# Optimization experiments

Measured on AMD Instinct MI355X. Metric: run time of the kernel, lower is better.

The kernel has to match this reference:

```python
import jax, jax.numpy as jnp
import numpy as np

B, L, H, E = 4, 2048, 16, 64  # batch, seq, heads, head_dim (S=L, D=E)


def setup_inputs() -> dict:
    key = jax.random.key(0)
    kq, kk, kv = jax.random.split(key, 3)
    queries = jax.random.normal(kq, (B, L, H, E), dtype=jnp.float32)
    keys = jax.random.normal(kk, (B, L, H, E), dtype=jnp.float32)
    values = jax.random.normal(kv, (B, L, H, E), dtype=jnp.float32)
    return {"queries": queries, "keys": keys, "values": values}


def reference(queries, keys, values):
    Bq, Lq, Hq, Eq = queries.shape
    scale = 1.0 / float(np.sqrt(Eq))
    # scores: [B, H, L, S]
    scores = jnp.einsum('blhe,bshe->bhls', queries, keys)
    # causal mask: forbid attending to future positions (strict upper triangle)
    causal = jnp.triu(jnp.ones((Lq, Lq), dtype=bool), k=1)
    scores = jnp.where(causal[None, None, :, :], -jnp.inf, scores)
    A = jax.nn.softmax(scale * scores, axis=-1)  # dropout p=0 -> identity
    V = jnp.einsum('bhls,bshd->blhd', A, values)  # [B, L, H, D]
    return V
```

## Files before the change

kernel.cpp:

```cpp
#include <hip/hip_runtime.h>
#include <hip/hip_bf16.h>

typedef short bs8 __attribute__((ext_vector_type(8)));
typedef short bs4 __attribute__((ext_vector_type(4)));
typedef float f32x4 __attribute__((ext_vector_type(4)));

#define B_ 4
#define L_ 2048
#define H_ 16
#define E_ 64
#define QT_ 128
#define KT_ 64
#define KSTR 72
#define PSTR 76
#define NEG_INF (-1e30f)
#define SCALE_LOG2E (0.125f * 1.44269504088896340736f)

__device__ __forceinline__ short bf16of(float x) {
  __hip_bfloat16 h = __float2bfloat16(x);
  return *reinterpret_cast<short*>(&h);
}

__global__ __launch_bounds__(256) void prep(const float* __restrict__ K,
                                            const float* __restrict__ V,
                                            short* __restrict__ Kb,
                                            short* __restrict__ Vt) {
  __shared__ unsigned int lt[64 * 35];
  const int tid = threadIdx.x;
  if (blockIdx.x < 1024) {
    size_t base = (size_t)blockIdx.x * 256 + tid;
#pragma unroll
    for (int i = 0; i < 8; ++i) {
      size_t g = base + (size_t)i * 262144;
      int e4 = g & 15;
      int h  = (g >> 4) & 15;
      int s  = (g >> 8) & 2047;
      int b  = (int)(g >> 19);
      float4 v = *(const float4*)(K + g * 4);
      bs4 o;
      o.x = bf16of(v.x); o.y = bf16of(v.y); o.z = bf16of(v.z); o.w = bf16of(v.w);
      *(bs4*)(Kb + (((size_t)(b * 16 + h) * L_ + s) * E_ + e4 * 4)) = o;
    }
  } else {
    int vb = blockIdx.x - 1024;
    int st = vb & 31, bh = vb >> 5;
    int b = bh >> 4, h = bh & 15;
    int s0 = st * 64;
#pragma unroll
    for (int i = 0; i < 2; ++i) {
      int idx = i * 256 + tid;
      int sp = idx >> 4;
      int e4 = idx & 15;
      const float* p0 = V + (((size_t)b * L_ + s0 + 2 * sp) * H_ + h) * E_ + e4 * 4;
      float4 v0 = *(const float4*)p0;
      float4 v1 = *(const float4*)(p0 + H_ * E_);
      unsigned u;
      u = (unsigned short)bf16of(v0.x) | ((unsigned)(unsigned short)bf16of(v1.x) << 16);
      lt[(e4 * 4 + 0) * 35 + sp] = u;
      u = (unsigned short)bf16of(v0.y) | ((unsigned)(unsigned short)bf16of(v1.y) << 16);
      lt[(e4 * 4 + 1) * 35 + sp] = u;
      u = (unsigned short)bf16of(v0.z) | ((unsigned)(unsigned short)bf16of(v1.z) << 16);
      lt[(e4 * 4 + 2) * 35 + sp] = u;
      u = (unsigned short)bf16of(v0.w) | ((unsigned)(unsigned short)bf16of(v1.w) << 16);
      lt[(e4 * 4 + 3) * 35 + sp] = u;
    }
    __syncthreads();
#pragma unroll
    for (int i = 0; i < 2; ++i) {
      int idx = i * 256 + tid;
      int e  = idx >> 3;
      int s8 = idx & 7;
      uint4 o;
      o.x = lt[e * 35 + s8 * 4 + 0];
      o.y = lt[e * 35 + s8 * 4 + 1];
      o.z = lt[e * 35 + s8 * 4 + 2];
      o.w = lt[e * 35 + s8 * 4 + 3];
      *(uint4*)(Vt + ((size_t)bh * E_ + e) * L_ + s0 + 8 * s8) = o;
    }
  }
}

__global__ __launch_bounds__(256, 2) void flash_fwd(const float* __restrict__ Q,
                                                    const short* __restrict__ Kb,
                                                    const short* __restrict__ Vt,
                                                    float* __restrict__ O) {
  const int p  = blockIdx.x;
  const int bh = blockIdx.y;
  const int b = bh >> 4, h = bh & 15;
  const int tid = threadIdx.x;
  const int w = tid >> 6;
  const int lane = tid & 63;
  const int quad = lane >> 4;
  const int l16 = lane & 15;

  __shared__ short ldsK[KT_ * KSTR];
  __shared__ short ldsV[E_ * KSTR];
  __shared__ short ldsP[QT_ * PSTR];

  const short* KbBase = Kb + (size_t)bh * L_ * E_;
  const short* VtBase = Vt + (size_t)bh * E_ * L_;

  const int sr = tid >> 3;
  const int sc = (tid & 7) * 8;

  bs8 bOne;
  {
    short one = (l16 == 0) ? (short)0x3F80 : (short)0;
#pragma unroll
    for (int j = 0; j < 8; ++j) bOne[j] = one;
  }

  for (int phase = 0; phase < 2; ++phase) {
    const int qt = phase ? (15 - p) : p;
    const int q0 = qt * QT_;
    const int nkt = 2 * qt + 2;

    bs8 aQ[2][2];
#pragma unroll
    for (int st = 0; st < 2; ++st) {
      const int q = q0 + w * 32 + st * 16 + l16;
      const float* qp = Q + (((size_t)b * L_ + q) * H_ + h) * E_ + quad * 8;
#pragma unroll
      for (int c = 0; c < 2; ++c) {
        float4 f0 = *(const float4*)(qp + c * 32);
        float4 f1 = *(const float4*)(qp + c * 32 + 4);
        bs8 a;
        a[0] = bf16of(f0.x * SCALE_LOG2E); a[1] = bf16of(f0.y * SCALE_LOG2E);
        a[2] = bf16of(f0.z * SCALE_LOG2E); a[3] = bf16of(f0.w * SCALE_LOG2E);
        a[4] = bf16of(f1.x * SCALE_LOG2E); a[5] = bf16of(f1.y * SCALE_LOG2E);
        a[6] = bf16of(f1.z * SCALE_LOG2E); a[7] = bf16of(f1.w * SCALE_LOG2E);
        aQ[st][c] = a;
      }
    }

    f32x4 accO[2][4];
    f32x4 accL[2];
#pragma unroll
    for (int st = 0; st < 2; ++st) {
      accL[st] = (f32x4){0.f, 0.f, 0.f, 0.f};
#pragma unroll
      for (int nt = 0; nt < 4; ++nt) accO[st][nt] = (f32x4){0.f, 0.f, 0.f, 0.f};
    }

    bs8 pfK[2], pfV[2];
#pragma unroll
    for (int i = 0; i < 2; ++i) {
      pfK[i] = *(const bs8*)(KbBase + (size_t)(sr + 32 * i) * E_ + sc);
      pfV[i] = *(const bs8*)(VtBase + (size_t)(sr + 32 * i) * L_ + sc);
    }

    for (int kt = 0; kt < nkt; ++kt) {
      const int k0 = kt * KT_;
      __syncthreads();

#pragma unroll
      for (int i = 0; i < 2; ++i) {
        *(bs8*)&ldsK[(sr + 32 * i) * KSTR + sc] = pfK[i];
        *(bs8*)&ldsV[(sr + 32 * i) * KSTR + sc] = pfV[i];
      }
      if (kt + 1 < nkt) {
        const int kn = k0 + KT_;
#pragma unroll
        for (int i = 0; i < 2; ++i) {
          pfK[i] = *(const bs8*)(KbBase + (size_t)(kn + sr + 32 * i) * E_ + sc);
          pfV[i] = *(const bs8*)(VtBase + (size_t)(sr + 32 * i) * L_ + kn + sc);
        }
      }
      __syncthreads();

      bool act[2];
      act[0] = (k0 <= q0 + w * 32 + 15);
      act[1] = (k0 <= q0 + w * 32 + 31);

      f32x4 sA[2][4];
#pragma unroll
      for (int nt = 0; nt < 4; ++nt) {
        bs8 bK0 = *(const bs8*)&ldsK[(nt * 16 + l16) * KSTR + quad * 8];
        bs8 bK1 = *(const bs8*)&ldsK[(nt * 16 + l16) * KSTR + 32 + quad * 8];
#pragma unroll
        for (int st = 0; st < 2; ++st) {
          if (act[st]) {
            f32x4 acc = (f32x4){0.f, 0.f, 0.f, 0.f};
            acc = __builtin_amdgcn_mfma_f32_16x16x32_bf16(aQ[st][0], bK0, acc, 0, 0, 0);
            acc = __builtin_amdgcn_mfma_f32_16x16x32_bf16(aQ[st][1], bK1, acc, 0, 0, 0);
            sA[st][nt] = acc;
          }
        }
      }

#pragma unroll
      for (int st = 0; st < 2; ++st) {
        const int sbase = q0 + w * 32 + st * 16;
        if (act[st] && (k0 + KT_ - 1 > sbase)) {
          const int qb = sbase + quad * 4;
#pragma unroll
          for (int nt = 0; nt < 4; ++nt) {
            int key = k0 + nt * 16 + l16;
#pragma unroll
            for (int r = 0; r < 4; ++r)
              if (key > qb + r) sA[st][nt][r] = NEG_INF;
          }
        }
      }

#pragma unroll
      for (int st = 0; st < 2; ++st) {
        if (act[st]) {
          const int rowb = w * 32 + st * 16 + quad * 4;
#pragma unroll
          for (int nt = 0; nt < 4; ++nt)
#pragma unroll
            for (int r = 0; r < 4; ++r)
              ldsP[(rowb + r) * PSTR + nt * 16 + l16] = bf16of(exp2f(sA[st][nt][r]));
        }
      }

      __threadfence_block();

      bs8 aP[2][2];
#pragma unroll
      for (int st = 0; st < 2; ++st) {
        if (act[st]) {
          const int rowa = w * 32 + st * 16 + l16;
#pragma unroll
          for (int c = 0; c < 2; ++c)
            aP[st][c] = *(const bs8*)&ldsP[rowa * PSTR + c * 32 + quad * 8];
          accL[st] = __builtin_amdgcn_mfma_f32_16x16x32_bf16(aP[st][0], bOne, accL[st], 0, 0, 0);
          accL[st] = __builtin_amdgcn_mfma_f32_16x16x32_bf16(aP[st][1], bOne, accL[st], 0, 0, 0);
        }
      }
#pragma unroll
      for (int nt = 0; nt < 4; ++nt) {
        bs8 bV0 = *(const bs8*)&ldsV[(nt * 16 + l16) * KSTR + quad * 8];
        bs8 bV1 = *(const bs8*)&ldsV[(nt * 16 + l16) * KSTR + 32 + quad * 8];
#pragma unroll
        for (int st = 0; st < 2; ++st) {
          if (act[st]) {
            accO[st][nt] = __builtin_amdgcn_mfma_f32_16x16x32_bf16(aP[st][0], bV0, accO[st][nt], 0, 0, 0);
            accO[st][nt] = __builtin_amdgcn_mfma_f32_16x16x32_bf16(aP[st][1], bV1, accO[st][nt], 0, 0, 0);
          }
        }
      }
    }

#pragma unroll
    for (int st = 0; st < 2; ++st) {
      float inv[4];
#pragma unroll
      for (int r = 0; r < 4; ++r)
        inv[r] = 1.f / __shfl(accL[st][r], lane & 48, 64);
#pragma unroll
      for (int nt = 0; nt < 4; ++nt) {
        const int q = q0 + w * 32 + st * 16 + quad * 4;
        const int d = nt * 16 + l16;
        float* op = O + (((size_t)b * L_ + q) * H_ + h) * E_ + d;
#pragma unroll
        for (int r = 0; r < 4; ++r)
          op[(size_t)r * H_ * E_] = accO[st][nt][r] * inv[r];
      }
    }
  }
}

extern "C" void kernel_launch(void* const* d_in, const int* in_sizes, int n_in,
                              void* d_out, int out_size, void* d_ws, size_t ws_size,
                              hipStream_t stream) {
  (void)in_sizes; (void)n_in; (void)out_size; (void)ws_size;
  const float* Q = (const float*)d_in[0];
  const float* K = (const float*)d_in[1];
  const float* V = (const float*)d_in[2];
  float* Out = (float*)d_out;
  short* Kb = (short*)d_ws;
  short* Vt = Kb + (size_t)B_ * H_ * L_ * E_;

  prep<<<1024 + 2048, 256, 0, stream>>>(K, V, Kb, Vt);
  flash_fwd<<<dim3(8, 64), 256, 0, stream>>>(Q, Kb, Vt, Out);
}
```

Measured before the change: 200.7 us.

## Compute transposed S=K·Q so row sums and P stores vectorize; widen K prep

```diff
diff --git a/kernel.cpp b/kernel.cpp
--- a/kernel.cpp
+++ b/kernel.cpp
@@ -12,13 +12,17 @@
 #define QT_ 128
 #define KT_ 64
 #define KSTR 72
-#define PSTR 76
+#define PSTR 72
 #define NEG_INF (-1e30f)
 #define SCALE_LOG2E (0.125f * 1.44269504088896340736f)
 
 __device__ __forceinline__ short bf16of(float x) {
   __hip_bfloat16 h = __float2bfloat16(x);
   return *reinterpret_cast<short*>(&h);
+}
+__device__ __forceinline__ unsigned pk2(float a, float b) {
+  return (unsigned)(unsigned short)bf16of(a) |
+         ((unsigned)(unsigned short)bf16of(b) << 16);
 }
 
 __global__ __launch_bounds__(256) void prep(const float* __restrict__ K,
@@ -27,22 +31,24 @@
                                             short* __restrict__ Vt) {
   __shared__ unsigned int lt[64 * 35];
   const int tid = threadIdx.x;
-  if (blockIdx.x < 1024) {
+  if (blockIdx.x < 2048) {
     size_t base = (size_t)blockIdx.x * 256 + tid;
 #pragma unroll
-    for (int i = 0; i < 8; ++i) {
-      size_t g = base + (size_t)i * 262144;
-      int e4 = g & 15;
-      int h  = (g >> 4) & 15;
-      int s  = (g >> 8) & 2047;
-      int b  = (int)(g >> 19);
-      float4 v = *(const float4*)(K + g * 4);
-      bs4 o;
-      o.x = bf16of(v.x); o.y = bf16of(v.y); o.z = bf16of(v.z); o.w = bf16of(v.w);
-      *(bs4*)(Kb + (((size_t)(b * 16 + h) * L_ + s) * E_ + e4 * 4)) = o;
+    for (int i = 0; i < 2; ++i) {
+      size_t u = base + (size_t)i * 524288;
+      int e8 = u & 7;
+      int h  = (u >> 3) & 15;
+      int s  = (u >> 7) & 2047;
+      int b  = (int)(u >> 18);
+      float4 f0 = *(const float4*)(K + u * 8);
+      float4 f1 = *(const float4*)(K + u * 8 + 4);
+      bs8 o;
+      o[0] = bf16of(f0.x); o[1] = bf16of(f0.y); o[2] = bf16of(f0.z); o[3] = bf16of(f0.w);
+      o[4] = bf16of(f1.x); o[5] = bf16of(f1.y); o[6] = bf16of(f1.z); o[7] = bf16of(f1.w);
+      *(bs8*)(Kb + (((size_t)(b * 16 + h) * L_ + s) * E_ + e8 * 8)) = o;
     }
   } else {
-    int vb = blockIdx.x - 1024;
+    int vb = blockIdx.x - 2048;
     int st = vb & 31, bh = vb >> 5;
     int b = bh >> 4, h = bh & 15;
     int s0 = st * 64;
@@ -54,15 +60,10 @@
       const float* p0 = V + (((size_t)b * L_ + s0 + 2 * sp) * H_ + h) * E_ + e4 * 4;
       float4 v0 = *(const float4*)p0;
       float4 v1 = *(const float4*)(p0 + H_ * E_);
-      unsigned u;
-      u = (unsigned short)bf16of(v0.x) | ((unsigned)(unsigned short)bf16of(v1.x) << 16);
-      lt[(e4 * 4 + 0) * 35 + sp] = u;
-      u = (unsigned short)bf16of(v0.y) | ((unsigned)(unsigned short)bf16of(v1.y) << 16);
-      lt[(e4 * 4 + 1) * 35 + sp] = u;
-      u = (unsigned short)bf16of(v0.z) | ((unsigned)(unsigned short)bf16of(v1.z) << 16);
-      lt[(e4 * 4 + 2) * 35 + sp] = u;
-      u = (unsigned short)bf16of(v0.w) | ((unsigned)(unsigned short)bf16of(v1.w) << 16);
-      lt[(e4 * 4 + 3) * 35 + sp] = u;
+      lt[(e4 * 4 + 0) * 35 + sp] = pk2(v0.x, v1.x);
+      lt[(e4 * 4 + 1) * 35 + sp] = pk2(v0.y, v1.y);
+      lt[(e4 * 4 + 2) * 35 + sp] = pk2(v0.z, v1.z);
+      lt[(e4 * 4 + 3) * 35 + sp] = pk2(v0.w, v1.w);
     }
     __syncthreads();
 #pragma unroll
@@ -103,13 +104,6 @@
   const int sr = tid >> 3;
   const int sc = (tid & 7) * 8;
 
-  bs8 bOne;
-  {
-    short one = (l16 == 0) ? (short)0x3F80 : (short)0;
-#pragma unroll
-    for (int j = 0; j < 8; ++j) bOne[j] = one;
-  }
-
   for (int phase = 0; phase < 2; ++phase) {
     const int qt = phase ? (15 - p) : p;
     const int q0 = qt * QT_;
@@ -134,10 +128,10 @@
     }
 
     f32x4 accO[2][4];
-    f32x4 accL[2];
+    float accLp[2];
 #pragma unroll
     for (int st = 0; st < 2; ++st) {
-      accL[st] = (f32x4){0.f, 0.f, 0.f, 0.f};
+      accLp[st] = 0.f;
 #pragma unroll
       for (int nt = 0; nt < 4; ++nt) accO[st][nt] = (f32x4){0.f, 0.f, 0.f, 0.f};
     }
@@ -168,76 +162,69 @@
       }
       __syncthreads();
 
-      bool act[2];
-      act[0] = (k0 <= q0 + w * 32 + 15);
-      act[1] = (k0 <= q0 + w * 32 + 31);
-
-      f32x4 sA[2][4];
-#pragma unroll
-      for (int nt = 0; nt < 4; ++nt) {
-        bs8 bK0 = *(const bs8*)&ldsK[(nt * 16 + l16) * KSTR + quad * 8];
-        bs8 bK1 = *(const bs8*)&ldsK[(nt * 16 + l16) * KSTR + 32 + quad * 8];
+      bool act0 = (k0 <= q0 + w * 32 + 15);
+      bool act1 = (k0 <= q0 + w * 32 + 31);
+
+      if (act1) {
+        bs8 aK0[4], aK1[4];
+#pragma unroll
+        for (int mt = 0; mt < 4; ++mt) {
+          aK0[mt] = *(const bs8*)&ldsK[(mt * 16 + l16) * KSTR + quad * 8];
+          aK1[mt] = *(const bs8*)&ldsK[(mt * 16 + l16) * KSTR + 32 + quad * 8];
+        }
+
 #pragma unroll
         for (int st = 0; st < 2; ++st) {
-          if (act[st]) {
-            f32x4 acc = (f32x4){0.f, 0.f, 0.f, 0.f};
-            acc = __builtin_amdgcn_mfma_f32_16x16x32_bf16(aQ[st][0], bK0, acc, 0, 0, 0);
-            acc = __builtin_amdgcn_mfma_f32_16x16x32_bf16(aQ[st][1], bK1, acc, 0, 0, 0);
-            sA[st][nt] = acc;
+          bool act = st ? act1 : act0;
+          if (act) {
+            const int qg = q0 + w * 32 + st * 16 + l16;
+            const bool diag = (k0 + KT_ - 1 > q0 + w * 32 + st * 16);
+            float rs = 0.f;
+#pragma unroll
+            for (int mt = 0; mt < 4; ++mt) {
+              f32x4 acc = (f32x4){0.f, 0.f, 0.f, 0.f};
+              acc = __builtin_amdgcn_mfma_f32_16x16x32_bf16(aK0[mt], aQ[st][0], acc, 0, 0, 0);
+              acc = __builtin_amdgcn_mfma_f32_16x16x32_bf16(aK1[mt], aQ[st][1], acc, 0, 0, 0);
+              if (diag) {
+                const int kb = k0 + mt * 16 + quad * 4;
+#pragma unroll
+                for (int r = 0; r < 4; ++r)
+                  if (kb + r > qg) acc[r] = NEG_INF;
+              }
+              float p0 = exp2f(acc[0]), p1 = exp2f(acc[1]);
+              float p2 = exp2f(acc[2]), p3 = exp2f(acc[3]);
+              rs += (p0 + p1) + (p2 + p3);
+              uint2 pw;
+              pw.x = pk2(p0, p1);
+              pw.y = pk2(p2, p3);
+              *(uint2*)&ldsP[(w * 32 + st * 16 + l16) * PSTR + mt * 16 + quad * 4] = pw;
+            }
+            accLp[st] += rs;
           }
         }
-      }
-
-#pragma unroll
-      for (int st = 0; st < 2; ++st) {
-        const int sbase = q0 + w * 32 + st * 16;
-        if (act[st] && (k0 + KT_ - 1 > sbase)) {
-          const int qb = sbase + quad * 4;
-#pragma unroll
-          for (int nt = 0; nt < 4; ++nt) {
-            int key = k0 + nt * 16 + l16;
-#pragma unroll
-            for (int r = 0; r < 4; ++r)
-              if (key > qb + r) sA[st][nt][r] = NEG_INF;
+
+        __threadfence_block();
+
+        bs8 aP[2][2];
+#pragma unroll
+        for (int st = 0; st < 2; ++st) {
+          if (st ? act1 : act0) {
+            const int rowa = w * 32 + st * 16 + l16;
+#pragma unroll
+            for (int c = 0; c < 2; ++c)
+              aP[st][c] = *(const bs8*)&ldsP[rowa * PSTR + c * 32 + quad * 8];
           }
         }
-      }
-
-#pragma unroll
-      for (int st = 0; st < 2; ++st) {
-        if (act[st]) {
-          const int rowb = w * 32 + st * 16 + quad * 4;
-#pragma unroll
-          for (int nt = 0; nt < 4; ++nt)
-#pragma unroll
-            for (int r = 0; r < 4; ++r)
-              ldsP[(rowb + r) * PSTR + nt * 16 + l16] = bf16of(exp2f(sA[st][nt][r]));
-        }
-      }
-
-      __threadfence_block();
-
-      bs8 aP[2][2];
-#pragma unroll
-      for (int st = 0; st < 2; ++st) {
-        if (act[st]) {
-          const int rowa = w * 32 + st * 16 + l16;
-#pragma unroll
-          for (int c = 0; c < 2; ++c)
-            aP[st][c] = *(const bs8*)&ldsP[rowa * PSTR + c * 32 + quad * 8];
-          accL[st] = __builtin_amdgcn_mfma_f32_16x16x32_bf16(aP[st][0], bOne, accL[st], 0, 0, 0);
-          accL[st] = __builtin_amdgcn_mfma_f32_16x16x32_bf16(aP[st][1], bOne, accL[st], 0, 0, 0);
-        }
-      }
-#pragma unroll
-      for (int nt = 0; nt < 4; ++nt) {
-        bs8 bV0 = *(const bs8*)&ldsV[(nt * 16 + l16) * KSTR + quad * 8];
-        bs8 bV1 = *(const bs8*)&ldsV[(nt * 16 + l16) * KSTR + 32 + quad * 8];
-#pragma unroll
-        for (int st = 0; st < 2; ++st) {
-          if (act[st]) {
-            accO[st][nt] = __builtin_amdgcn_mfma_f32_16x16x32_bf16(aP[st][0], bV0, accO[st][nt], 0, 0, 0);
-            accO[st][nt] = __builtin_amdgcn_mfma_f32_16x16x32_bf16(aP[st][1], bV1, accO[st][nt], 0, 0, 0);
+#pragma unroll
+        for (int nt = 0; nt < 4; ++nt) {
+          bs8 bV0 = *(const bs8*)&ldsV[(nt * 16 + l16) * KSTR + quad * 8];
+          bs8 bV1 = *(const bs8*)&ldsV[(nt * 16 + l16) * KSTR + 32 + quad * 8];
+#pragma unroll
+          for (int st = 0; st < 2; ++st) {
+            if (st ? act1 : act0) {
+              accO[st][nt] = __builtin_amdgcn_mfma_f32_16x16x32_bf16(aP[st][0], bV0, accO[st][nt], 0, 0, 0);
+              accO[st][nt] = __builtin_amdgcn_mfma_f32_16x16x32_bf16(aP[st][1], bV1, accO[st][nt], 0, 0, 0);
+            }
           }
         }
       }
@@ -245,10 +232,13 @@
 
 #pragma unroll
     for (int st = 0; st < 2; ++st) {
+      float lf = accLp[st];
+      lf += __shfl_xor(lf, 16, 64);
+      lf += __shfl_xor(lf, 32, 64);
       float inv[4];
 #pragma unroll
       for (int r = 0; r < 4; ++r)
-        inv[r] = 1.f / __shfl(accL[st][r], lane & 48, 64);
+        inv[r] = 1.f / __shfl(lf, quad * 4 + r, 64);
 #pragma unroll
       for (int nt = 0; nt < 4; ++nt) {
         const int q = q0 + w * 32 + st * 16 + quad * 4;
@@ -273,6 +263,6 @@
   short* Kb = (short*)d_ws;
   short* Vt = Kb + (size_t)B_ * H_ * L_ * E_;
 
-  prep<<<1024 + 2048, 256, 0, stream>>>(K, V, Kb, Vt);
+  prep<<<4096, 256, 0, stream>>>(K, V, Kb, Vt);
   flash_fwd<<<dim3(8, 64), 256, 0, stream>>>(Q, Kb, Vt, Out);
 }
```

Result: no change. 200.8 us (+0.1%).
